# Optimization experiments

Measured on AMD Instinct MI355X. Metric: run time of the kernel, lower is better.

## Reference

```python
import jax, jax.numpy as jnp
import numpy as np

N = 10000      # nodes
E = 160000     # edges (before self loops)
G = 16         # graphs in batch
H = 4          # attention heads
F = 128        # hidden_dim (per-head out channels)
DIN = 64       # input_dim
NEG_SLOPE = 0.2


def setup_inputs() -> dict:
    key = jax.random.key(0)
    ks = jax.random.split(key, 20)
    x = jax.random.normal(ks[0], (N, DIN), jnp.float32)
    edge_index = jax.random.randint(ks[1], (2, E), 0, N, jnp.int32)
    batch = jnp.sort(jax.random.randint(ks[2], (N,), 0, G, jnp.int32))

    def p(k, shape, scale):
        return (jax.random.normal(k, shape, jnp.float32) * scale).astype(jnp.float32)

    ins = [DIN, H * F, H * F]
    params = {}
    for i in range(3):
        d = ins[i]
        params[f"W{i}"] = p(ks[3 + 4 * i], (d, H * F), (2.0 / (d + F)) ** 0.5)
        params[f"as{i}"] = p(ks[4 + 4 * i], (H, F), 0.1)
        params[f"ad{i}"] = p(ks[5 + 4 * i], (H, F), 0.1)
        bdim = H * F if i < 2 else F
        params[f"b{i}"] = jnp.zeros((bdim,), jnp.float32)
    params["Wr1"] = p(ks[15], (F, F), (2.0 / (2 * F)) ** 0.5)
    params["br1"] = jnp.zeros((F,), jnp.float32)
    params["Wr2"] = p(ks[16], (F, 2 * F), (2.0 / (3 * F)) ** 0.5)
    params["br2"] = jnp.zeros((2 * F,), jnp.float32)
    return {"x": x, "edge_index": edge_index, "batch": batch, **params}


def gat_layer(x, src, dst, W, a_s, a_d, b, concat):
    """PyG-style GATConv (eval mode, self loops already in src/dst)."""
    n = x.shape[0]
    h = (x @ W).reshape(n, H, F)                      # [N,H,F]
    e = jax.nn.leaky_relu(((h * a_s).sum(-1))[src] + ((h * a_d).sum(-1))[dst], NEG_SLOPE)  # [E,H]
    m = jax.ops.segment_max(e, dst, num_segments=n)   # segment softmax over dst
    w = jnp.exp(e - m[dst])
    denom = jax.ops.segment_sum(w, dst, num_segments=n)
    alpha = w / denom[dst]                            # [E,H]
    out = jax.ops.segment_sum(alpha[:, :, None] * h[src], dst, num_segments=n)  # [N,H,F]
    out = out.reshape(n, H * F) if concat else out.mean(axis=1)
    return out + b


def reference(x, edge_index, batch, W0, as0, ad0, b0, W1, as1, ad1, b1,
              W2, as2, ad2, b2, Wr1, br1, Wr2, br2):
    n = x.shape[0]
    loops = jnp.arange(n, dtype=edge_index.dtype)     # add_self_loops (PyG default)
    src = jnp.concatenate([edge_index[0], loops])
    dst = jnp.concatenate([edge_index[1], loops])
    h = jax.nn.relu(gat_layer(x, src, dst, W0, as0, ad0, b0, True))
    h = jax.nn.relu(gat_layer(h, src, dst, W1, as1, ad1, b1, True))
    h = gat_layer(h, src, dst, W2, as2, ad2, b2, False)   # [N,F]
    # global mean pool over graphs
    sums = jax.ops.segment_sum(h, batch, num_segments=G)
    cnt = jax.ops.segment_sum(jnp.ones((n, 1), h.dtype), batch, num_segments=G)
    g = sums / jnp.maximum(cnt, 1.0)                   # [G,F]
    z = jax.nn.relu(g @ Wr1 + br1)
    return z @ Wr2 + br2                               # [G,256]
```

## Files before the change

kernel.cpp:

```cpp
#include <hip/hip_runtime.h>
#include <hip/hip_bf16.h>
#include <math.h>

constexpr int NN  = 10000;
constexpr int NE  = 160000;
constexpr int GG  = 16;
constexpr int HH  = 4;
constexpr int FF  = 128;
constexpr int HF  = 512;

typedef __attribute__((ext_vector_type(8))) short bf16x8;
typedef __attribute__((ext_vector_type(4))) float f32x4;

__device__ inline short f2bf(float v) {
    __hip_bfloat16 h = __float2bfloat16(v);
    return *reinterpret_cast<short*>(&h);
}
__device__ inline float bf2f(short s) {
    __hip_bfloat16 h = *reinterpret_cast<__hip_bfloat16*>(&s);
    return __bfloat162float(h);
}

__global__ __launch_bounds__(256) void zero_kernel(int* __restrict__ counts,
                                                   float* __restrict__ sums) {
    int i = blockIdx.x * 256 + threadIdx.x;
    if (i < NN) counts[i] = 0;
    if (i < GG * FF) sums[i] = 0.f;
}

__global__ __launch_bounds__(256) void prep_count(const float* __restrict__ x,
                                                  short* __restrict__ xb,
                                                  const float* __restrict__ W0,
                                                  const float* __restrict__ W1,
                                                  const float* __restrict__ W2,
                                                  short* __restrict__ T0,
                                                  short* __restrict__ T1,
                                                  short* __restrict__ T2,
                                                  const int* __restrict__ ei,
                                                  int* __restrict__ counts) {
    int z = blockIdx.z;
    int tid = threadIdx.x;
    int bid = blockIdx.y * 16 + blockIdx.x;
    if (z == 3) {
        for (int i = bid * 256 + tid; i < NN * 64; i += 256 * 256)
            xb[i] = f2bf(x[i]);
        return;
    }
    if (z == 4) {
        int g = bid * 256 + tid;
        for (int e = g; e < NE; e += 256 * 256)
            atomicAdd(&counts[ei[NE + e]], 1);
        return;
    }
    const float* W = (z == 0) ? W0 : (z == 1) ? W1 : W2;
    short* T = (z == 0) ? T0 : (z == 1) ? T1 : T2;
    int K = (z == 0) ? 64 : HF;
    int bn = blockIdx.x * 32, bk = blockIdx.y * 32;
    if (bk >= K) return;
    __shared__ float tile[32][33];
    int tx = tid & 31, ty = tid >> 5;
    for (int r = ty; r < 32; r += 8) {
        int k = bk + r, n = bn + tx;
        tile[r][tx] = W[(size_t)k * HF + n];
    }
    __syncthreads();
    for (int r = ty; r < 32; r += 8) {
        int n = bn + r, k = bk + tx;
        T[(size_t)n * K + k] = f2bf(tile[tx][r]);
    }
}

__global__ __launch_bounds__(1024) void scan_offsets(const int* __restrict__ counts,
                                                     int* __restrict__ offsets,
                                                     int* __restrict__ cursor) {
    __shared__ int wsum[16];
    __shared__ int carry;
    int tid = threadIdx.x, lane = tid & 63, wv = tid >> 6;
    if (tid == 0) carry = 0;
    __syncthreads();
    for (int base = 0; base < NN; base += 1024) {
        int i = base + tid;
        int v = (i < NN) ? counts[i] : 0;
        int x = v;
#pragma unroll
        for (int st = 1; st < 64; st <<= 1) {
            int t = __shfl_up(x, st);
            if (lane >= st) x += t;
        }
        if (lane == 63) wsum[wv] = x;
        __syncthreads();
        if (tid == 0) {
            int s = carry;
            for (int k2 = 0; k2 < 16; k2++) { int t = wsum[k2]; wsum[k2] = s; s += t; }
            carry = s;
        }
        __syncthreads();
        int excl = wsum[wv] + x - v;
        if (i < NN) { offsets[i] = excl; cursor[i] = excl; }
        __syncthreads();
    }
    if (tid == 0) offsets[NN] = carry;
}

__global__ void scatter_edges(const int* __restrict__ ei, int* __restrict__ cursor,
                              int* __restrict__ adj) {
    int e = blockIdx.x * 256 + threadIdx.x;
    if (e < NE) {
        int dst = ei[NE + e];
        int pos = atomicAdd(&cursor[dst], 1);
        adj[pos] = ei[e];
    }
}

__global__ __launch_bounds__(256) void gemm_attn(const short* __restrict__ A,
                                                 const short* __restrict__ B,
                                                 short* __restrict__ Cb,
                                                 float* __restrict__ es,
                                                 float* __restrict__ ed,
                                                 const float* __restrict__ a_s,
                                                 const float* __restrict__ a_d,
                                                 int M, int K) {
    constexpr int BM = 64, BK = 32, LDT = BK + 8;
    __shared__ short As[BM][LDT];
    __shared__ short Bh[FF][LDT];
    __shared__ float s_red[4][BM][2];
    int tid = threadIdx.x;
    int wave = tid >> 6, lane = tid & 63;
    int fr = lane & 15, fq = lane >> 4;
    int bm = blockIdx.x * BM;
    int head = blockIdx.y;
    int bn = head * FF;
    int arow = tid >> 2, acol = (tid & 3) * 8;
    int brow = tid >> 1, bcol = (tid & 1) * 16;
    f32x4 acc[4][2] = {};
    for (int k0 = 0; k0 < K; k0 += BK) {
        {
            int row = bm + arow;
            bf16x8 va = {};
            if (row < M) va = *(const bf16x8*)&A[(size_t)row * K + k0 + acol];
            *(bf16x8*)&As[arow][acol] = va;
            const short* bsh = &B[(size_t)(bn + brow) * K + k0 + bcol];
            *(bf16x8*)&Bh[brow][bcol]     = *(const bf16x8*)bsh;
            *(bf16x8*)&Bh[brow][bcol + 8] = *(const bf16x8*)(bsh + 8);
        }
        __syncthreads();
        bf16x8 af[4], bh[2];
#pragma unroll
        for (int m = 0; m < 4; m++)
            af[m] = *(const bf16x8*)&As[m * 16 + fr][fq * 8];
#pragma unroll
        for (int n = 0; n < 2; n++)
            bh[n] = *(const bf16x8*)&Bh[wave * 32 + n * 16 + fr][fq * 8];
#pragma unroll
        for (int m = 0; m < 4; m++)
#pragma unroll
            for (int n = 0; n < 2; n++)
                acc[m][n] = __builtin_amdgcn_mfma_f32_16x16x32_bf16(af[m], bh[n], acc[m][n], 0, 0, 0);
        __syncthreads();
    }
    float asv[2], adv[2];
#pragma unroll
    for (int n = 0; n < 2; n++) {
        int c = wave * 32 + n * 16 + fr;
        asv[n] = a_s[head * FF + c];
        adv[n] = a_d[head * FF + c];
    }
#pragma unroll
    for (int m = 0; m < 4; m++) {
#pragma unroll
        for (int j = 0; j < 4; j++) {
            float ps = 0.f, pd = 0.f;
#pragma unroll
            for (int n = 0; n < 2; n++) {
                float v = acc[m][n][j];
                ps += v * asv[n];
                pd += v * adv[n];
            }
#pragma unroll
            for (int o = 1; o < 16; o <<= 1) {
                ps += __shfl_xor(ps, o);
                pd += __shfl_xor(pd, o);
            }
            int rloc = m * 16 + fq * 4 + j;
            if (fr == 0) { s_red[wave][rloc][0] = ps; s_red[wave][rloc][1] = pd; }
            int row = bm + rloc;
            if (row < M) {
#pragma unroll
                for (int n = 0; n < 2; n++)
                    Cb[(size_t)row * HF + bn + wave * 32 + n * 16 + fr] = f2bf(acc[m][n][j]);
            }
        }
    }
    __syncthreads();
    if (tid < BM) {
        int row = bm + tid;
        if (row < M) {
            es[row * 4 + head] = s_red[0][tid][0] + s_red[1][tid][0] +
                                 s_red[2][tid][0] + s_red[3][tid][0];
            ed[row * 4 + head] = s_red[0][tid][1] + s_red[1][tid][1] +
                                 s_red[2][tid][1] + s_red[3][tid][1];
        }
    }
}

template <int MODE>
__global__ __launch_bounds__(256) void gat_aggregate(const short* __restrict__ h,
                                                     const float* __restrict__ es,
                                                     const float* __restrict__ ed,
                                                     const int* __restrict__ offsets,
                                                     const int* __restrict__ adj,
                                                     const float* __restrict__ bias,
                                                     float* __restrict__ outf,
                                                     short* __restrict__ outb) {
    constexpr int CAP = 64;
    __shared__ int s_src[4][CAP];
    __shared__ float s_wt[4][4][CAP];
    int tid = threadIdx.x, w = tid >> 6, lane = tid & 63;
    int n = blockIdx.x * 4 + w;
    int row0 = offsets[n];
    int deg = offsets[n + 1] - row0;
    int tot = min(deg + 1, CAP);
    if (lane < tot)
        s_src[w][lane] = (lane < deg) ? adj[row0 + lane] : n;
    float4 edv = *(const float4*)&ed[n * 4];
    float mx0 = -1e30f, mx1 = -1e30f, mx2 = -1e30f, mx3 = -1e30f;
    if (lane < tot) {
        int s = s_src[w][lane];
        float4 e4 = *(const float4*)&es[s * 4];
        float e0 = e4.x + edv.x; e0 = (e0 >= 0.f) ? e0 : 0.2f * e0;
        float e1 = e4.y + edv.y; e1 = (e1 >= 0.f) ? e1 : 0.2f * e1;
        float e2 = e4.z + edv.z; e2 = (e2 >= 0.f) ? e2 : 0.2f * e2;
        float e3 = e4.w + edv.w; e3 = (e3 >= 0.f) ? e3 : 0.2f * e3;
        s_wt[w][0][lane] = e0; s_wt[w][1][lane] = e1;
        s_wt[w][2][lane] = e2; s_wt[w][3][lane] = e3;
        mx0 = e0; mx1 = e1; mx2 = e2; mx3 = e3;
    }
#pragma unroll
    for (int o = 1; o < 64; o <<= 1) {
        mx0 = fmaxf(mx0, __shfl_xor(mx0, o));
        mx1 = fmaxf(mx1, __shfl_xor(mx1, o));
        mx2 = fmaxf(mx2, __shfl_xor(mx2, o));
        mx3 = fmaxf(mx3, __shfl_xor(mx3, o));
    }
    float s0 = 0.f, s1 = 0.f, s2 = 0.f, s3 = 0.f;
    if (lane < tot) {
        float v0 = __expf(s_wt[w][0][lane] - mx0); s_wt[w][0][lane] = v0; s0 = v0;
        float v1 = __expf(s_wt[w][1][lane] - mx1); s_wt[w][1][lane] = v1; s1 = v1;
        float v2 = __expf(s_wt[w][2][lane] - mx2); s_wt[w][2][lane] = v2; s2 = v2;
        float v3 = __expf(s_wt[w][3][lane] - mx3); s_wt[w][3][lane] = v3; s3 = v3;
    }
#pragma unroll
    for (int o = 1; o < 64; o <<= 1) {
        s0 += __shfl_xor(s0, o); s1 += __shfl_xor(s1, o);
        s2 += __shfl_xor(s2, o); s3 += __shfl_xor(s3, o);
    }
    __syncthreads();
    int head = lane >> 4;
    float rd = 1.f / ((head == 0) ? s0 : (head == 1) ? s1 : (head == 2) ? s2 : s3);
    float acc[8] = {};
    const short* hbase = h + lane * 8;
    for (int i = 0; i < tot; i++) {
        int s = s_src[w][i];
        float wt = s_wt[w][head][i];
        bf16x8 hv = *(const bf16x8*)&hbase[(size_t)s * HF];
#pragma unroll
        for (int k = 0; k < 8; k++) acc[k] += wt * bf2f(hv[k]);
    }
#pragma unroll
    for (int k = 0; k < 8; k++) acc[k] *= rd;
    if (MODE == 0) {
        int c = lane * 8;
        float4 b0 = *(const float4*)&bias[c];
        float4 b1 = *(const float4*)&bias[c + 4];
        bf16x8 o;
        o[0] = f2bf(fmaxf(acc[0] + b0.x, 0.f));
        o[1] = f2bf(fmaxf(acc[1] + b0.y, 0.f));
        o[2] = f2bf(fmaxf(acc[2] + b0.z, 0.f));
        o[3] = f2bf(fmaxf(acc[3] + b0.w, 0.f));
        o[4] = f2bf(fmaxf(acc[4] + b1.x, 0.f));
        o[5] = f2bf(fmaxf(acc[5] + b1.y, 0.f));
        o[6] = f2bf(fmaxf(acc[6] + b1.z, 0.f));
        o[7] = f2bf(fmaxf(acc[7] + b1.w, 0.f));
        *(bf16x8*)&outb[(size_t)n * HF + c] = o;
    } else {
#pragma unroll
        for (int k = 0; k < 8; k++) {
            acc[k] += __shfl_xor(acc[k], 16);
            acc[k] += __shfl_xor(acc[k], 32);
        }
        if (lane < 16) {
            int c = lane * 8;
#pragma unroll
            for (int k = 0; k < 8; k++)
                outf[(size_t)n * FF + c + k] = 0.25f * acc[k] + bias[c + k];
        }
    }
}

__global__ __launch_bounds__(128) void pool_kernel(const float* __restrict__ h2,
                                                   const int* __restrict__ batch,
                                                   float* __restrict__ sums) {
    int f = threadIdx.x;
    int start = blockIdx.x * 64;
    float acc = 0.f;
    int curg = -1;
    for (int i = 0; i < 64; i++) {
        int node = start + i;
        if (node >= NN) break;
        int g = batch[node];
        if (g != curg) {
            if (curg >= 0) atomicAdd(&sums[curg * FF + f], acc);
            acc = 0.f;
            curg = g;
        }
        acc += h2[(size_t)node * FF + f];
    }
    if (curg >= 0) atomicAdd(&sums[curg * FF + f], acc);
}

__global__ __launch_bounds__(256) void mlp_kernel(const float* __restrict__ sums,
                                                  const int* __restrict__ batch,
                                                  const float* __restrict__ Wr1,
                                                  const float* __restrict__ br1,
                                                  const float* __restrict__ Wr2,
                                                  const float* __restrict__ br2,
                                                  float* __restrict__ out) {
    int g = blockIdx.x, t = threadIdx.x;
    __shared__ float gv[128];
    __shared__ float z[128];
    __shared__ float cinv;
    if (t == 0) {
        auto lb = [&](int key) {
            int lo = 0, hi = NN;
            while (lo < hi) { int mid = (lo + hi) >> 1; if (batch[mid] < key) lo = mid + 1; else hi = mid; }
            return lo;
        };
        int cnt = lb(g + 1) - lb(g);
        cinv = 1.0f / fmaxf((float)cnt, 1.0f);
    }
    __syncthreads();
    if (t < 128) gv[t] = sums[g * FF + t] * cinv;
    __syncthreads();
    if (t < 128) {
        float a = br1[t];
        for (int k = 0; k < 128; k++) a += gv[k] * Wr1[k * 128 + t];
        z[t] = fmaxf(a, 0.f);
    }
    __syncthreads();
    {
        float a = br2[t];
        for (int k = 0; k < 128; k++) a += z[k] * Wr2[k * 256 + t];
        out[g * 256 + t] = a;
    }
}

extern "C" void kernel_launch(void* const* d_in, const int* in_sizes, int n_in,
                              void* d_out, int out_size, void* d_ws, size_t ws_size,
                              hipStream_t stream) {
    const float* x    = (const float*)d_in[0];
    const int*   ei   = (const int*)d_in[1];
    const int*   batch= (const int*)d_in[2];
    const float* W0   = (const float*)d_in[3];
    const float* as0  = (const float*)d_in[4];
    const float* ad0  = (const float*)d_in[5];
    const float* b0   = (const float*)d_in[6];
    const float* W1   = (const float*)d_in[7];
    const float* as1  = (const float*)d_in[8];
    const float* ad1  = (const float*)d_in[9];
    const float* b1   = (const float*)d_in[10];
    const float* W2   = (const float*)d_in[11];
    const float* as2  = (const float*)d_in[12];
    const float* ad2  = (const float*)d_in[13];
    const float* b2   = (const float*)d_in[14];
    const float* Wr1  = (const float*)d_in[15];
    const float* br1  = (const float*)d_in[16];
    const float* Wr2  = (const float*)d_in[17];
    const float* br2  = (const float*)d_in[18];
    float* out = (float*)d_out;

    char* p = (char*)d_ws;
    auto alloc = [&](size_t bytes) {
        char* r = p;
        p += (bytes + 255) / 256 * 256;
        return r;
    };
    short* hA      = (short*)alloc((size_t)NN * HF * 2);
    short* hB      = (short*)alloc((size_t)NN * HF * 2);
    float* h2      = (float*)alloc((size_t)NN * FF * 4);
    short* xb      = (short*)alloc((size_t)NN * 64 * 2);
    short* T0      = (short*)alloc((size_t)HF * 64 * 2);
    short* T1      = (short*)alloc((size_t)HF * HF * 2);
    short* T2      = (short*)alloc((size_t)HF * HF * 2);
    float* es      = (float*)alloc((size_t)NN * HH * 4);
    float* ed      = (float*)alloc((size_t)NN * HH * 4);
    int*   counts  = (int*)alloc((size_t)NN * 4);
    int*   offsets = (int*)alloc((size_t)(NN + 1) * 4);
    int*   cursor  = (int*)alloc((size_t)NN * 4);
    int*   adj     = (int*)alloc((size_t)NE * 4);
    float* sums    = (float*)alloc((size_t)GG * FF * 4);

    zero_kernel<<<(NN + 255) / 256, 256, 0, stream>>>(counts, sums);

    prep_count<<<dim3(16, 16, 5), 256, 0, stream>>>(x, xb, W0, W1, W2, T0, T1, T2,
                                                    ei, counts);

    scan_offsets<<<1, 1024, 0, stream>>>(counts, offsets, cursor);
    scatter_edges<<<(NE + 255) / 256, 256, 0, stream>>>(ei, cursor, adj);

    dim3 ggemm((NN + 63) / 64, HH);

    gemm_attn<<<ggemm, 256, 0, stream>>>(xb, T0, hA, es, ed, as0, ad0, NN, 64);
    gat_aggregate<0><<<NN / 4, 256, 0, stream>>>(hA, es, ed, offsets, adj, b0, nullptr, hB);

    gemm_attn<<<ggemm, 256, 0, stream>>>(hB, T1, hA, es, ed, as1, ad1, NN, HF);
    gat_aggregate<0><<<NN / 4, 256, 0, stream>>>(hA, es, ed, offsets, adj, b1, nullptr, hB);

    gemm_attn<<<ggemm, 256, 0, stream>>>(hB, T2, hA, es, ed, as2, ad2, NN, HF);
    gat_aggregate<1><<<NN / 4, 256, 0, stream>>>(hA, es, ed, offsets, adj, b2, h2, nullptr);

    pool_kernel<<<(NN + 63) / 64, 128, 0, stream>>>(h2, batch, sums);
    mlp_kernel<<<GG, 256, 0, stream>>>(sums, batch, Wr1, br1, Wr2, br2, out);
}
```

Before: 199.5 us.

## Fuse graph preprocessing and pooling into fewer kernel launches

Builds the destination histogram and prefix scan in a single one-block kernel using shared-memory atomics. The edge scatter is folded into the weight-transpose/conversion kernel, and that kernel's input conversion is vectorised. Mean pooling is merged into the MLP kernel, which now sums each graph's contiguous node range directly instead of using global atomics. This cuts the launch count from 13 to 9 and drops the zero-init pass. The cost is a serial single-block histogram over 160k edges and a pooling step that runs on only 16 blocks.

```diff
diff --git a/kernel.cpp b/kernel.cpp
--- a/kernel.cpp
+++ b/kernel.cpp
@@ -21,35 +21,72 @@
     return __bfloat162float(h);
 }
 
-__global__ __launch_bounds__(256) void zero_kernel(int* __restrict__ counts,
-                                                   float* __restrict__ sums) {
-    int i = blockIdx.x * 256 + threadIdx.x;
-    if (i < NN) counts[i] = 0;
-    if (i < GG * FF) sums[i] = 0.f;
-}
-
-__global__ __launch_bounds__(256) void prep_count(const float* __restrict__ x,
-                                                  short* __restrict__ xb,
-                                                  const float* __restrict__ W0,
-                                                  const float* __restrict__ W1,
-                                                  const float* __restrict__ W2,
-                                                  short* __restrict__ T0,
-                                                  short* __restrict__ T1,
-                                                  short* __restrict__ T2,
-                                                  const int* __restrict__ ei,
-                                                  int* __restrict__ counts) {
+__global__ __launch_bounds__(1024) void histo_scan(const int* __restrict__ ei,
+                                                   int* __restrict__ offsets,
+                                                   int* __restrict__ cursor) {
+    __shared__ int hist[NN];
+    __shared__ int wsum[16];
+    __shared__ int carry;
+    int tid = threadIdx.x, lane = tid & 63, wv = tid >> 6;
+    for (int i = tid; i < NN; i += 1024) hist[i] = 0;
+    if (tid == 0) carry = 0;
+    __syncthreads();
+    for (int e = tid; e < NE; e += 1024) atomicAdd(&hist[ei[NE + e]], 1);
+    __syncthreads();
+    for (int base = 0; base < NN; base += 1024) {
+        int i = base + tid;
+        int v = (i < NN) ? hist[i] : 0;
+        int x = v;
+#pragma unroll
+        for (int st = 1; st < 64; st <<= 1) {
+            int t = __shfl_up(x, st);
+            if (lane >= st) x += t;
+        }
+        if (lane == 63) wsum[wv] = x;
+        __syncthreads();
+        if (tid == 0) {
+            int s = carry;
+            for (int k2 = 0; k2 < 16; k2++) { int t = wsum[k2]; wsum[k2] = s; s += t; }
+            carry = s;
+        }
+        __syncthreads();
+        int excl = wsum[wv] + x - v;
+        if (i < NN) { offsets[i] = excl; cursor[i] = excl; }
+        __syncthreads();
+    }
+    if (tid == 0) offsets[NN] = carry;
+}
+
+__global__ __launch_bounds__(256) void prep_scatter(const float* __restrict__ x,
+                                                    short* __restrict__ xb,
+                                                    const float* __restrict__ W0,
+                                                    const float* __restrict__ W1,
+                                                    const float* __restrict__ W2,
+                                                    short* __restrict__ T0,
+                                                    short* __restrict__ T1,
+                                                    short* __restrict__ T2,
+                                                    const int* __restrict__ ei,
+                                                    int* __restrict__ cursor,
+                                                    int* __restrict__ adj) {
     int z = blockIdx.z;
     int tid = threadIdx.x;
     int bid = blockIdx.y * 16 + blockIdx.x;
     if (z == 3) {
-        for (int i = bid * 256 + tid; i < NN * 64; i += 256 * 256)
-            xb[i] = f2bf(x[i]);
+        const float4* x4 = (const float4*)x;
+        for (int i = bid * 256 + tid; i < NN * 16; i += 256 * 256) {
+            float4 v = x4[i];
+            short4 o;
+            o.x = f2bf(v.x); o.y = f2bf(v.y); o.z = f2bf(v.z); o.w = f2bf(v.w);
+            *(short4*)&xb[i * 4] = o;
+        }
         return;
     }
     if (z == 4) {
-        int g = bid * 256 + tid;
-        for (int e = g; e < NE; e += 256 * 256)
-            atomicAdd(&counts[ei[NE + e]], 1);
+        for (int e = bid * 256 + tid; e < NE; e += 256 * 256) {
+            int dst = ei[NE + e];
+            int pos = atomicAdd(&cursor[dst], 1);
+            adj[pos] = ei[e];
+        }
         return;
     }
     const float* W = (z == 0) ? W0 : (z == 1) ? W1 : W2;
@@ -67,48 +104,6 @@
     for (int r = ty; r < 32; r += 8) {
         int n = bn + r, k = bk + tx;
         T[(size_t)n * K + k] = f2bf(tile[tx][r]);
-    }
-}
-
-__global__ __launch_bounds__(1024) void scan_offsets(const int* __restrict__ counts,
-                                                     int* __restrict__ offsets,
-                                                     int* __restrict__ cursor) {
-    __shared__ int wsum[16];
-    __shared__ int carry;
-    int tid = threadIdx.x, lane = tid & 63, wv = tid >> 6;
-    if (tid == 0) carry = 0;
-    __syncthreads();
-    for (int base = 0; base < NN; base += 1024) {
-        int i = base + tid;
-        int v = (i < NN) ? counts[i] : 0;
-        int x = v;
-#pragma unroll
-        for (int st = 1; st < 64; st <<= 1) {
-            int t = __shfl_up(x, st);
-            if (lane >= st) x += t;
-        }
-        if (lane == 63) wsum[wv] = x;
-        __syncthreads();
-        if (tid == 0) {
-            int s = carry;
-            for (int k2 = 0; k2 < 16; k2++) { int t = wsum[k2]; wsum[k2] = s; s += t; }
-            carry = s;
-        }
-        __syncthreads();
-        int excl = wsum[wv] + x - v;
-        if (i < NN) { offsets[i] = excl; cursor[i] = excl; }
-        __syncthreads();
-    }
-    if (tid == 0) offsets[NN] = carry;
-}
-
-__global__ void scatter_edges(const int* __restrict__ ei, int* __restrict__ cursor,
-                              int* __restrict__ adj) {
-    int e = blockIdx.x * 256 + threadIdx.x;
-    if (e < NE) {
-        int dst = ei[NE + e];
-        int pos = atomicAdd(&cursor[dst], 1);
-        adj[pos] = ei[e];
     }
 }
 
@@ -297,49 +292,38 @@
     }
 }
 
-__global__ __launch_bounds__(128) void pool_kernel(const float* __restrict__ h2,
-                                                   const int* __restrict__ batch,
-                                                   float* __restrict__ sums) {
-    int f = threadIdx.x;
-    int start = blockIdx.x * 64;
-    float acc = 0.f;
-    int curg = -1;
-    for (int i = 0; i < 64; i++) {
-        int node = start + i;
-        if (node >= NN) break;
-        int g = batch[node];
-        if (g != curg) {
-            if (curg >= 0) atomicAdd(&sums[curg * FF + f], acc);
-            acc = 0.f;
-            curg = g;
-        }
-        acc += h2[(size_t)node * FF + f];
-    }
-    if (curg >= 0) atomicAdd(&sums[curg * FF + f], acc);
-}
-
-__global__ __launch_bounds__(256) void mlp_kernel(const float* __restrict__ sums,
-                                                  const int* __restrict__ batch,
-                                                  const float* __restrict__ Wr1,
-                                                  const float* __restrict__ br1,
-                                                  const float* __restrict__ Wr2,
-                                                  const float* __restrict__ br2,
-                                                  float* __restrict__ out) {
+__global__ __launch_bounds__(256) void mlp_pool(const float* __restrict__ h2,
+                                                const int* __restrict__ batch,
+                                                const float* __restrict__ Wr1,
+                                                const float* __restrict__ br1,
+                                                const float* __restrict__ Wr2,
+                                                const float* __restrict__ br2,
+                                                float* __restrict__ out) {
     int g = blockIdx.x, t = threadIdx.x;
+    __shared__ float spart[2][128];
     __shared__ float gv[128];
     __shared__ float z[128];
-    __shared__ float cinv;
+    __shared__ int s_lo, s_hi;
     if (t == 0) {
         auto lb = [&](int key) {
             int lo = 0, hi = NN;
             while (lo < hi) { int mid = (lo + hi) >> 1; if (batch[mid] < key) lo = mid + 1; else hi = mid; }
             return lo;
         };
-        int cnt = lb(g + 1) - lb(g);
-        cinv = 1.0f / fmaxf((float)cnt, 1.0f);
-    }
-    __syncthreads();
-    if (t < 128) gv[t] = sums[g * FF + t] * cinv;
+        s_lo = lb(g);
+        s_hi = lb(g + 1);
+    }
+    __syncthreads();
+    int lo = s_lo, hi = s_hi;
+    int f = t & 127, part = t >> 7;
+    float acc = 0.f;
+    for (int i = lo + part; i < hi; i += 2) acc += h2[(size_t)i * FF + f];
+    spart[part][f] = acc;
+    __syncthreads();
+    if (t < 128) {
+        float c = fmaxf((float)(hi - lo), 1.0f);
+        gv[t] = (spart[0][t] + spart[1][t]) / c;
+    }
     __syncthreads();
     if (t < 128) {
         float a = br1[t];
@@ -393,19 +377,14 @@
     short* T2      = (short*)alloc((size_t)HF * HF * 2);
     float* es      = (float*)alloc((size_t)NN * HH * 4);
     float* ed      = (float*)alloc((size_t)NN * HH * 4);
-    int*   counts  = (int*)alloc((size_t)NN * 4);
     int*   offsets = (int*)alloc((size_t)(NN + 1) * 4);
     int*   cursor  = (int*)alloc((size_t)NN * 4);
     int*   adj     = (int*)alloc((size_t)NE * 4);
-    float* sums    = (float*)alloc((size_t)GG * FF * 4);
-
-    zero_kernel<<<(NN + 255) / 256, 256, 0, stream>>>(counts, sums);
-
-    prep_count<<<dim3(16, 16, 5), 256, 0, stream>>>(x, xb, W0, W1, W2, T0, T1, T2,
-                                                    ei, counts);
-
-    scan_offsets<<<1, 1024, 0, stream>>>(counts, offsets, cursor);
-    scatter_edges<<<(NE + 255) / 256, 256, 0, stream>>>(ei, cursor, adj);
+
+    histo_scan<<<1, 1024, 0, stream>>>(ei, offsets, cursor);
+
+    prep_scatter<<<dim3(16, 16, 5), 256, 0, stream>>>(x, xb, W0, W1, W2, T0, T1, T2,
+                                                      ei, cursor, adj);
 
     dim3 ggemm((NN + 63) / 64, HH);
 
@@ -418,6 +397,5 @@
     gemm_attn<<<ggemm, 256, 0, stream>>>(hB, T2, hA, es, ed, as2, ad2, NN, HF);
     gat_aggregate<1><<<NN / 4, 256, 0, stream>>>(hA, es, ed, offsets, adj, b2, h2, nullptr);
 
-    pool_kernel<<<(NN + 63) / 64, 128, 0, stream>>>(h2, batch, sums);
-    mlp_kernel<<<GG, 256, 0, stream>>>(sums, batch, Wr1, br1, Wr2, br2, out);
-}
+    mlp_pool<<<GG, 256, 0, stream>>>(h2, batch, Wr1, br1, Wr2, br2, out);
+}
```

Measured after the change: 279.7 us. 1.4x slower.

## Merge CSR histogram and scan into one kernel, fuse scatter into prep

Applied to the files above, without the earlier changes.

Four preprocessing launches (zero, prep+count, scan, scatter) become two. A single 1024-thread block builds the destination histogram in shared memory with LDS atomics, scans it, and zeroes the pooling sums. The edge scatter now runs as a slice of the weight-transpose/convert kernel, and the x-to-bf16 conversion is vectorised with float4 loads. This removes launches and the global count buffer, but the histogram now runs on one workgroup, so 160k atomic adds are serialised on a single CU.

```diff
diff --git a/kernel.cpp b/kernel.cpp
--- a/kernel.cpp
+++ b/kernel.cpp
@@ -21,35 +21,74 @@
     return __bfloat162float(h);
 }
 
-__global__ __launch_bounds__(256) void zero_kernel(int* __restrict__ counts,
+__global__ __launch_bounds__(1024) void histo_scan(const int* __restrict__ ei,
+                                                   int* __restrict__ offsets,
+                                                   int* __restrict__ cursor,
                                                    float* __restrict__ sums) {
-    int i = blockIdx.x * 256 + threadIdx.x;
-    if (i < NN) counts[i] = 0;
-    if (i < GG * FF) sums[i] = 0.f;
-}
-
-__global__ __launch_bounds__(256) void prep_count(const float* __restrict__ x,
-                                                  short* __restrict__ xb,
-                                                  const float* __restrict__ W0,
-                                                  const float* __restrict__ W1,
-                                                  const float* __restrict__ W2,
-                                                  short* __restrict__ T0,
-                                                  short* __restrict__ T1,
-                                                  short* __restrict__ T2,
-                                                  const int* __restrict__ ei,
-                                                  int* __restrict__ counts) {
+    __shared__ int hist[NN];
+    __shared__ int wsum[16];
+    __shared__ int carry;
+    int tid = threadIdx.x, lane = tid & 63, wv = tid >> 6;
+    for (int i = tid; i < NN; i += 1024) hist[i] = 0;
+    for (int i = tid; i < GG * FF; i += 1024) sums[i] = 0.f;
+    if (tid == 0) carry = 0;
+    __syncthreads();
+    for (int e = tid; e < NE; e += 1024) atomicAdd(&hist[ei[NE + e]], 1);
+    __syncthreads();
+    for (int base = 0; base < NN; base += 1024) {
+        int i = base + tid;
+        int v = (i < NN) ? hist[i] : 0;
+        int x = v;
+#pragma unroll
+        for (int st = 1; st < 64; st <<= 1) {
+            int t = __shfl_up(x, st);
+            if (lane >= st) x += t;
+        }
+        if (lane == 63) wsum[wv] = x;
+        __syncthreads();
+        if (tid == 0) {
+            int s = carry;
+            for (int k2 = 0; k2 < 16; k2++) { int t = wsum[k2]; wsum[k2] = s; s += t; }
+            carry = s;
+        }
+        __syncthreads();
+        int excl = wsum[wv] + x - v;
+        if (i < NN) { offsets[i] = excl; cursor[i] = excl; }
+        __syncthreads();
+    }
+    if (tid == 0) offsets[NN] = carry;
+}
+
+__global__ __launch_bounds__(256) void prep_scatter(const float* __restrict__ x,
+                                                    short* __restrict__ xb,
+                                                    const float* __restrict__ W0,
+                                                    const float* __restrict__ W1,
+                                                    const float* __restrict__ W2,
+                                                    short* __restrict__ T0,
+                                                    short* __restrict__ T1,
+                                                    short* __restrict__ T2,
+                                                    const int* __restrict__ ei,
+                                                    int* __restrict__ cursor,
+                                                    int* __restrict__ adj) {
     int z = blockIdx.z;
     int tid = threadIdx.x;
     int bid = blockIdx.y * 16 + blockIdx.x;
     if (z == 3) {
-        for (int i = bid * 256 + tid; i < NN * 64; i += 256 * 256)
-            xb[i] = f2bf(x[i]);
+        const float4* x4 = (const float4*)x;
+        for (int i = bid * 256 + tid; i < NN * 16; i += 256 * 256) {
+            float4 v = x4[i];
+            short4 o;
+            o.x = f2bf(v.x); o.y = f2bf(v.y); o.z = f2bf(v.z); o.w = f2bf(v.w);
+            *(short4*)&xb[i * 4] = o;
+        }
         return;
     }
     if (z == 4) {
-        int g = bid * 256 + tid;
-        for (int e = g; e < NE; e += 256 * 256)
-            atomicAdd(&counts[ei[NE + e]], 1);
+        for (int e = bid * 256 + tid; e < NE; e += 256 * 256) {
+            int dst = ei[NE + e];
+            int pos = atomicAdd(&cursor[dst], 1);
+            adj[pos] = ei[e];
+        }
         return;
     }
     const float* W = (z == 0) ? W0 : (z == 1) ? W1 : W2;
@@ -67,48 +106,6 @@
     for (int r = ty; r < 32; r += 8) {
         int n = bn + r, k = bk + tx;
         T[(size_t)n * K + k] = f2bf(tile[tx][r]);
-    }
-}
-
-__global__ __launch_bounds__(1024) void scan_offsets(const int* __restrict__ counts,
-                                                     int* __restrict__ offsets,
-                                                     int* __restrict__ cursor) {
-    __shared__ int wsum[16];
-    __shared__ int carry;
-    int tid = threadIdx.x, lane = tid & 63, wv = tid >> 6;
-    if (tid == 0) carry = 0;
-    __syncthreads();
-    for (int base = 0; base < NN; base += 1024) {
-        int i = base + tid;
-        int v = (i < NN) ? counts[i] : 0;
-        int x = v;
-#pragma unroll
-        for (int st = 1; st < 64; st <<= 1) {
-            int t = __shfl_up(x, st);
-            if (lane >= st) x += t;
-        }
-        if (lane == 63) wsum[wv] = x;
-        __syncthreads();
-        if (tid == 0) {
-            int s = carry;
-            for (int k2 = 0; k2 < 16; k2++) { int t = wsum[k2]; wsum[k2] = s; s += t; }
-            carry = s;
-        }
-        __syncthreads();
-        int excl = wsum[wv] + x - v;
-        if (i < NN) { offsets[i] = excl; cursor[i] = excl; }
-        __syncthreads();
-    }
-    if (tid == 0) offsets[NN] = carry;
-}
-
-__global__ void scatter_edges(const int* __restrict__ ei, int* __restrict__ cursor,
-                              int* __restrict__ adj) {
-    int e = blockIdx.x * 256 + threadIdx.x;
-    if (e < NE) {
-        int dst = ei[NE + e];
-        int pos = atomicAdd(&cursor[dst], 1);
-        adj[pos] = ei[e];
     }
 }
 
@@ -393,19 +390,15 @@
     short* T2      = (short*)alloc((size_t)HF * HF * 2);
     float* es      = (float*)alloc((size_t)NN * HH * 4);
     float* ed      = (float*)alloc((size_t)NN * HH * 4);
-    int*   counts  = (int*)alloc((size_t)NN * 4);
     int*   offsets = (int*)alloc((size_t)(NN + 1) * 4);
     int*   cursor  = (int*)alloc((size_t)NN * 4);
     int*   adj     = (int*)alloc((size_t)NE * 4);
     float* sums    = (float*)alloc((size_t)GG * FF * 4);
 
-    zero_kernel<<<(NN + 255) / 256, 256, 0, stream>>>(counts, sums);
-
-    prep_count<<<dim3(16, 16, 5), 256, 0, stream>>>(x, xb, W0, W1, W2, T0, T1, T2,
-                                                    ei, counts);
-
-    scan_offsets<<<1, 1024, 0, stream>>>(counts, offsets, cursor);
-    scatter_edges<<<(NE + 255) / 256, 256, 0, stream>>>(ei, cursor, adj);
+    histo_scan<<<1, 1024, 0, stream>>>(ei, offsets, cursor, sums);
+
+    prep_scatter<<<dim3(16, 16, 5), 256, 0, stream>>>(x, xb, W0, W1, W2, T0, T1, T2,
+                                                      ei, cursor, adj);
 
     dim3 ggemm((NN + 63) / 64, HH);
 
```

New measurement: 221.3 us. 10.9% more time.
